# Performance work log

Measured on AMD Instinct MI355X. Metric: run time of the kernel, lower is better.

Reference implementation:

```python
import jax, jax.numpy as jnp
import numpy as np

G, B, C, H, W, D = 4, 1, 128, 32, 32, 32
STS = 4          # super_token_size (cubic)
N_ITER = 2
NUM_HEADS = 8
EPS = 1e-12


def _unfold3(x):
    """x: [..., H, W, D] -> [..., 27, H, W, D]; 3x3x3 neighborhood, zero pad."""
    *lead, h, w, d = x.shape
    xp = jnp.pad(x, [(0, 0)] * len(lead) + [(1, 1), (1, 1), (1, 1)])
    patches = [xp[..., i:i + h, j:j + w, l:l + d]
               for i in range(3) for j in range(3) for l in range(3)]
    return jnp.stack(patches, axis=-4)


def _fold3(x):
    """x: [..., 27, H, W, D] -> [..., H, W, D]; adjoint of _unfold3 (scatter-add)."""
    *lead, k27, h, w, d = x.shape
    out = jnp.zeros((*lead, h + 2, w + 2, d + 2), x.dtype)
    k = 0
    for i in range(3):
        for j in range(3):
            for l in range(3):
                out = out.at[..., i:i + h, j:j + w, l:l + d].add(x[..., k, :, :, :])
                k += 1
    return out[..., 1:h + 1, 1:w + 1, 1:d + 1]


def _attention_p(x, w_qkv, w_proj, b_proj):
    """Full self-attention over all voxels of x: [Bt, C, h, w, d]."""
    bt, c, hh, ww, dd = x.shape
    n = hh * ww * dd
    hd = c // NUM_HEADS
    xf = x.reshape(bt, c, n)
    qkv = jnp.einsum('oc,bcn->bon', w_qkv, xf)          # [Bt, 3C, N] (1x1 conv3d, no bias)
    q, k, v = jnp.split(qkv, 3, axis=1)
    q = q.reshape(bt * NUM_HEADS, hd, n) * (hd ** -0.5)
    k = k.reshape(bt * NUM_HEADS, hd, n)
    v = v.reshape(bt * NUM_HEADS, hd, n)
    attn = jax.nn.softmax(jnp.einsum('bcm,bcn->bmn', q, k), axis=-1)
    o = jnp.einsum('bmn,bcn->bcm', attn, v).reshape(bt, c, n)
    o = jnp.einsum('oc,bcn->bon', w_proj, o) + b_proj[None, :, None]
    return o.reshape(bt, c, hh, ww, dd)


def setup_inputs() -> dict:
    key = jax.random.key(0)
    k1, k2, k3, k4 = jax.random.split(key, 4)
    return {
        'x': jax.random.normal(k1, (G, B, C, H, W, D), jnp.float32),
        'w_qkv': jax.random.normal(k2, (3 * C, C), jnp.float32) * 0.02,
        'w_proj': jax.random.normal(k3, (C, C), jnp.float32) * 0.02,
        'b_proj': jax.random.normal(k4, (C,), jnp.float32) * 0.02,
    }


def reference(x, w_qkv, w_proj, b_proj):
    g, b, c, hH, wW, dD = x.shape
    bt = g * b
    xb = x.reshape(bt, c, hH, wW, dD)
    s = STS
    hh, ww, dd = hH // s, wW // s, dD // s
    m, p = hh * ww * dd, s ** 3
    scale = c ** -0.5

    blocks = xb.reshape(bt, c, hh, s, ww, s, dd, s)
    super_t = blocks.mean(axis=(3, 5, 7))                                   # [Bt,C,hh,ww,dd]
    pixel = blocks.transpose(0, 2, 4, 6, 3, 5, 7, 1).reshape(bt, m, p, c)    # [Bt,M,P,C]

    def _aff(st):
        su = _unfold3(st).reshape(bt, c, 27, m).transpose(0, 3, 1, 2)        # [Bt,M,C,27]
        return jax.nn.softmax(jnp.einsum('bmpc,bmck->bmpk', pixel, su) * scale, axis=-1)

    # iterative clustering (torch.no_grad in original)
    st = super_t
    aff = None
    asum = None
    for idx in range(N_ITER):
        aff = _aff(st)                                                       # [Bt,M,P,27]
        asum = _fold3(aff.sum(2).transpose(0, 2, 1).reshape(bt, 27, hh, ww, dd))[:, None]  # [Bt,1,hh,ww,dd]
        if idx < N_ITER - 1:
            stn = jnp.einsum('bmpc,bmpk->bmck', pixel, aff)                  # [Bt,M,C,27]
            stn = _fold3(stn.transpose(0, 2, 3, 1).reshape(bt, c, 27, hh, ww, dd))
            st = stn / (asum[:, 0][:, None] + EPS) if False else stn / (asum + EPS)
    aff = jax.lax.stop_gradient(aff)
    asum = jax.lax.stop_gradient(asum)

    st = jnp.einsum('bmpc,bmpk->bmck', pixel, aff)
    st = _fold3(st.transpose(0, 2, 3, 1).reshape(bt, c, 27, hh, ww, dd))
    st = st / (asum + EPS)                                                   # [Bt,C,hh,ww,dd]

    st = _attention_p(st, w_qkv, w_proj, b_proj)                             # refine

    su = _unfold3(st).reshape(bt, c, 27, m).transpose(0, 3, 1, 2)            # [Bt,M,C,27]
    pix = jnp.einsum('bmck,bmpk->bmcp', su, aff)                             # [Bt,M,C,P]
    out = pix.reshape(bt, hh, ww, dd, c, s, s, s).transpose(0, 4, 1, 5, 2, 6, 3, 7)
    out = out.reshape(bt, c, hH, wW, dD)
    return out.reshape(g, b, c, hH, wW, dD)
```

## Files before the change

kernel.cpp:

```cpp
#include <hip/hip_runtime.h>

#define BT 4
#define NC 128
#define MM 512
#define PP 64
#define K27 27
#define GSC 0.08838834764831845f
#define EPSF 1e-12f


__global__ __launch_bounds__(256) void k_pack(const float* __restrict__ x,
                                              float* __restrict__ px,
                                              float* __restrict__ st0p) {
    __shared__ float sl[128 * 36];
    const int blk = blockIdx.x & 255;
    const int phase = blockIdx.x >> 8;
    const int b = blk >> 6, gh = (blk >> 3) & 7, gw = blk & 7;
    const int tid = threadIdx.x;
    const int cL = tid >> 1, half = tid & 1;
    const int c4 = tid & 31, gd = tid >> 5;
    const int m = gh * 64 + gw * 8 + gd;
    float acc[4] = {0.f, 0.f, 0.f, 0.f};
    const size_t xbase = (size_t)b * NC * 32768 + (size_t)(gh * 4) * 1024 + (size_t)(gw * 4) * 32;

    for (int t = 0; t < 2; ++t) {
        const int ij = phase * 2 + t;
        const int i = ij >> 2, j = ij & 3;
        if (t) __syncthreads();
        const float* xp = x + xbase + (size_t)cL * 32768 + i * 1024 + j * 32 + half * 16;
#pragma unroll
        for (int q = 0; q < 4; ++q) {
            float4 v = *(const float4*)(xp + q * 4);
            *(float4*)&sl[cL * 36 + half * 16 + q * 4] = v;
        }
        __syncthreads();
        const float4 vq0 = *(const float4*)&sl[(c4 * 4 + 0) * 36 + gd * 4];
        const float4 vq1 = *(const float4*)&sl[(c4 * 4 + 1) * 36 + gd * 4];
        const float4 vq2 = *(const float4*)&sl[(c4 * 4 + 2) * 36 + gd * 4];
        const float4 vq3 = *(const float4*)&sl[(c4 * 4 + 3) * 36 + gd * 4];
        float* pb = px + ((size_t)(b * MM + m) * PP + (i * 16 + j * 4)) * NC + c4 * 4;
        *(float4*)(pb + 0 * NC) = make_float4(vq0.x, vq1.x, vq2.x, vq3.x);
        *(float4*)(pb + 1 * NC) = make_float4(vq0.y, vq1.y, vq2.y, vq3.y);
        *(float4*)(pb + 2 * NC) = make_float4(vq0.z, vq1.z, vq2.z, vq3.z);
        *(float4*)(pb + 3 * NC) = make_float4(vq0.w, vq1.w, vq2.w, vq3.w);
        acc[0] += vq0.x + vq0.y + vq0.z + vq0.w;
        acc[1] += vq1.x + vq1.y + vq1.z + vq1.w;
        acc[2] += vq2.x + vq2.y + vq2.z + vq2.w;
        acc[3] += vq3.x + vq3.y + vq3.z + vq3.w;
    }
    float4 a4 = make_float4(acc[0], acc[1], acc[2], acc[3]);
    a4.x *= (1.f / 64.f); a4.y *= (1.f / 64.f); a4.z *= (1.f / 64.f); a4.w *= (1.f / 64.f);
    *(float4*)&st0p[(size_t)phase * BT * MM * NC + (size_t)(b * MM + m) * NC + c4 * 4] = a4;
}

__global__ __launch_bounds__(128) void k_sum8(const float* __restrict__ st0p,
                                              float* __restrict__ st0) {
    const int row = blockIdx.x;
    const int c = threadIdx.x;
    const size_t idx = (size_t)row * NC + c;
    const size_t stride = (size_t)BT * MM * NC;
    float s = 0.f;
#pragma unroll
    for (int ph = 0; ph < 8; ++ph) s += st0p[ph * stride + idx];
    st0[idx] = s;
}

__global__ __launch_bounds__(256) void k_unpack(const float* __restrict__ pxo,
                                                float* __restrict__ out) {
    __shared__ float sl[128 * 36];
    const int blk = blockIdx.x & 255;
    const int phase = blockIdx.x >> 8;
    const int b = blk >> 6, gh = (blk >> 3) & 7, gw = blk & 7;
    const int tid = threadIdx.x;
    const int cL = tid >> 1, half = tid & 1;
    const int c4 = tid & 31, gd = tid >> 5;
    const int m = gh * 64 + gw * 8 + gd;
    const size_t obase = (size_t)b * NC * 32768 + (size_t)(gh * 4) * 1024 + (size_t)(gw * 4) * 32;

    for (int t = 0; t < 2; ++t) {
        const int ij = phase * 2 + t;
        const int i = ij >> 2, j = ij & 3;
        if (t) __syncthreads();
        const float* pb = pxo + ((size_t)(b * MM + m) * PP + (i * 16 + j * 4)) * NC + c4 * 4;
        const float4 w0 = *(const float4*)(pb + 0 * NC);
        const float4 w1 = *(const float4*)(pb + 1 * NC);
        const float4 w2 = *(const float4*)(pb + 2 * NC);
        const float4 w3 = *(const float4*)(pb + 3 * NC);
        *(float4*)&sl[(c4 * 4 + 0) * 36 + gd * 4] = make_float4(w0.x, w1.x, w2.x, w3.x);
        *(float4*)&sl[(c4 * 4 + 1) * 36 + gd * 4] = make_float4(w0.y, w1.y, w2.y, w3.y);
        *(float4*)&sl[(c4 * 4 + 2) * 36 + gd * 4] = make_float4(w0.z, w1.z, w2.z, w3.z);
        *(float4*)&sl[(c4 * 4 + 3) * 36 + gd * 4] = make_float4(w0.w, w1.w, w2.w, w3.w);
        __syncthreads();
        float* op = out + obase + (size_t)cL * 32768 + i * 1024 + j * 32 + half * 16;
#pragma unroll
        for (int q = 0; q < 4; ++q)
            *(float4*)(op + q * 4) = *(const float4*)&sl[cL * 36 + half * 16 + q * 4];
    }
}

template <int STORE_AFF>
__global__ __launch_bounds__(256) void k_iter(const float* __restrict__ px,
                                              const float* __restrict__ st,
                                              float* __restrict__ stn,
                                              float* __restrict__ affsum,
                                              float* __restrict__ affout) {
    __shared__ float pix[64 * 128];
    __shared__ float aff[64 * 28];
    const int tid = threadIdx.x;
    const int wg = blockIdx.x;
    const int b = wg >> 9;
    const int m = wg & (MM - 1);
    const int gh = m >> 6, gw = (m >> 3) & 7, gd = m & 7;

    const float* pxt = px + (size_t)wg * PP * NC;
    for (int t = tid; t < 2048; t += 256) {
        const int p = t >> 5, cb = t & 31;
        float4 v = *(const float4*)(pxt + t * 4);
        *(float4*)&pix[p * 128 + ((cb ^ (p & 7)) << 2)] = v;
    }

    const int kq = tid >> 6;
    const int kb = kq * 7;
    const int selfoff = (b * MM + m) * NC;
    int soff[7];
    int vmask = 0;
#pragma unroll
    for (int j = 0; j < 7; ++j) {
        const int k = kb + j;
        soff[j] = selfoff;
        if (k < K27) {
            const int i3 = k / 9, j3 = (k / 3) % 3, l3 = k % 3;
            const int mh = gh + i3 - 1, mw = gw + j3 - 1, md = gd + l3 - 1;
            if ((unsigned)mh < 8u && (unsigned)mw < 8u && (unsigned)md < 8u) {
                soff[j] = (b * MM + (mh * 64 + mw * 8 + md)) * NC;
                vmask |= (1 << j);
            }
        }
    }
    vmask = __builtin_amdgcn_readfirstlane(vmask);
    __syncthreads();

    {
        const int lane = tid & 63;
        const int pg = lane & 15, cseg = lane >> 4;
        float a00=0,a01=0,a02=0,a03=0,a04=0,a05=0,a06=0;
        float a10=0,a11=0,a12=0,a13=0,a14=0,a15=0,a16=0;
        float a20=0,a21=0,a22=0,a23=0,a24=0,a25=0,a26=0;
        float a30=0,a31=0,a32=0,a33=0,a34=0,a35=0,a36=0;
#pragma unroll 1
        for (int step = 0; step < 8; ++step) {
            const int cb = step * 4 + cseg;
            const int cb4 = cb * 4;
            const float4 sv0 = *(const float4*)(st + soff[0] + cb4);
            const float4 sv1 = *(const float4*)(st + soff[1] + cb4);
            const float4 sv2 = *(const float4*)(st + soff[2] + cb4);
            const float4 sv3 = *(const float4*)(st + soff[3] + cb4);
            const float4 sv4 = *(const float4*)(st + soff[4] + cb4);
            const float4 sv5 = *(const float4*)(st + soff[5] + cb4);
            const float4 sv6 = *(const float4*)(st + soff[6] + cb4);
            const float4 pv0 = *(const float4*)&pix[(pg +  0) * 128 + ((cb ^ ((pg +  0) & 7)) << 2)];
            const float4 pv1 = *(const float4*)&pix[(pg + 16) * 128 + ((cb ^ ((pg + 16) & 7)) << 2)];
            const float4 pv2 = *(const float4*)&pix[(pg + 32) * 128 + ((cb ^ ((pg + 32) & 7)) << 2)];
            const float4 pv3 = *(const float4*)&pix[(pg + 48) * 128 + ((cb ^ ((pg + 48) & 7)) << 2)];
#define DOT4(sv, A0, A1, A2, A3)                                          \
            A0 += pv0.x*sv.x + pv0.y*sv.y + pv0.z*sv.z + pv0.w*sv.w;      \
            A1 += pv1.x*sv.x + pv1.y*sv.y + pv1.z*sv.z + pv1.w*sv.w;      \
            A2 += pv2.x*sv.x + pv2.y*sv.y + pv2.z*sv.z + pv2.w*sv.w;      \
            A3 += pv3.x*sv.x + pv3.y*sv.y + pv3.z*sv.z + pv3.w*sv.w;
            DOT4(sv0, a00, a10, a20, a30)
            DOT4(sv1, a01, a11, a21, a31)
            DOT4(sv2, a02, a12, a22, a32)
            DOT4(sv3, a03, a13, a23, a33)
            DOT4(sv4, a04, a14, a24, a34)
            DOT4(sv5, a05, a15, a25, a35)
            DOT4(sv6, a06, a16, a26, a36)
#undef DOT4
        }
        if (!(vmask &  1)) { a00=0; a10=0; a20=0; a30=0; }
        if (!(vmask &  2)) { a01=0; a11=0; a21=0; a31=0; }
        if (!(vmask &  4)) { a02=0; a12=0; a22=0; a32=0; }
        if (!(vmask &  8)) { a03=0; a13=0; a23=0; a33=0; }
        if (!(vmask & 16)) { a04=0; a14=0; a24=0; a34=0; }
        if (!(vmask & 32)) { a05=0; a15=0; a25=0; a35=0; }
        if (!(vmask & 64)) { a06=0; a16=0; a26=0; a36=0; }
#define RED(v) v += __shfl_xor(v, 16); v += __shfl_xor(v, 32);
        RED(a00) RED(a01) RED(a02) RED(a03) RED(a04) RED(a05) RED(a06)
        RED(a10) RED(a11) RED(a12) RED(a13) RED(a14) RED(a15) RED(a16)
        RED(a20) RED(a21) RED(a22) RED(a23) RED(a24) RED(a25) RED(a26)
        RED(a30) RED(a31) RED(a32) RED(a33) RED(a34) RED(a35) RED(a36)
#undef RED
        if (cseg == 0) {
            float* r0 = &aff[(pg +  0) * 28 + kb];
            r0[0]=a00; r0[1]=a01; r0[2]=a02; r0[3]=a03; r0[4]=a04; r0[5]=a05; r0[6]=a06;
            float* r1 = &aff[(pg + 16) * 28 + kb];
            r1[0]=a10; r1[1]=a11; r1[2]=a12; r1[3]=a13; r1[4]=a14; r1[5]=a15; r1[6]=a16;
            float* r2 = &aff[(pg + 32) * 28 + kb];
            r2[0]=a20; r2[1]=a21; r2[2]=a22; r2[3]=a23; r2[4]=a24; r2[5]=a25; r2[6]=a26;
            float* r3 = &aff[(pg + 48) * 28 + kb];
            r3[0]=a30; r3[1]=a31; r3[2]=a32; r3[3]=a33; r3[4]=a34; r3[5]=a35; r3[6]=a36;
        }
    }
    __syncthreads();

    {
        const int p = tid >> 2, sub4 = tid & 3;
        const int k0 = sub4 * 7;
        float row[7];
        float mx = -1e30f;
#pragma unroll
        for (int t = 0; t < 7; ++t) {
            if (k0 + t < K27) {
                row[t] = aff[p * 28 + k0 + t] * GSC;
                mx = fmaxf(mx, row[t]);
            }
        }
        mx = fmaxf(mx, __shfl_xor(mx, 1));
        mx = fmaxf(mx, __shfl_xor(mx, 2));
        float s = 0.f;
#pragma unroll
        for (int t = 0; t < 7; ++t) {
            if (k0 + t < K27) {
                row[t] = __expf(row[t] - mx);
                s += row[t];
            }
        }
        s += __shfl_xor(s, 1);
        s += __shfl_xor(s, 2);
        const float inv = 1.f / s;
#pragma unroll
        for (int t = 0; t < 7; ++t)
            if (k0 + t < K27) aff[p * 28 + k0 + t] = row[t] * inv;
        if (sub4 == 3) aff[p * 28 + 27] = 0.f;
    }
    __syncthreads();

    if (tid < 216) {
        const int k = tid >> 3, seg = tid & 7;
        float s = 0.f;
#pragma unroll
        for (int pp = 0; pp < 8; ++pp) s += aff[(seg * 8 + pp) * 28 + k];
        s += __shfl_xor(s, 1);
        s += __shfl_xor(s, 2);
        s += __shfl_xor(s, 4);
        if (seg == 0) affsum[((size_t)b * K27 + k) * MM + m] = s;
    }
    if (STORE_AFF) {
        const size_t base = (size_t)(b * MM + m) * PP * K27;
        for (int t = tid; t < PP * K27; t += 256) {
            int p = t / K27, k = t - p * K27;
            affout[base + t] = aff[p * 28 + k];
        }
    }

    {
        const int kq2 = tid >> 5, cq = tid & 31;
        if (kq2 < 7) {
            float c00=0,c01=0,c02=0,c03=0;
            float c10=0,c11=0,c12=0,c13=0;
            float c20=0,c21=0,c22=0,c23=0;
            float c30=0,c31=0,c32=0,c33=0;
#pragma unroll 2
            for (int p = 0; p < 64; ++p) {
                float4 pv = *(const float4*)&pix[p * 128 + ((cq ^ (p & 7)) << 2)];
                float4 av = *(const float4*)&aff[p * 28 + kq2 * 4];
                c00 += av.x * pv.x; c01 += av.x * pv.y; c02 += av.x * pv.z; c03 += av.x * pv.w;
                c10 += av.y * pv.x; c11 += av.y * pv.y; c12 += av.y * pv.z; c13 += av.y * pv.w;
                c20 += av.z * pv.x; c21 += av.z * pv.y; c22 += av.z * pv.z; c23 += av.z * pv.w;
                c30 += av.w * pv.x; c31 += av.w * pv.y; c32 += av.w * pv.z; c33 += av.w * pv.w;
            }
            const int k0 = kq2 * 4;
#pragma unroll
            for (int q = 0; q < 4; ++q) {
                const int k = k0 + q;
                if (k < K27) {
                    const int i3 = k / 9, j3 = (k / 3) % 3, l3 = k % 3;
                    const int mh = gh + i3 - 1, mw = gw + j3 - 1, md = gd + l3 - 1;
                    if ((unsigned)mh < 8u && (unsigned)mw < 8u && (unsigned)md < 8u) {
                        float4 w4 = (q == 0) ? make_float4(c00, c01, c02, c03)
                                  : (q == 1) ? make_float4(c10, c11, c12, c13)
                                  : (q == 2) ? make_float4(c20, c21, c22, c23)
                                             : make_float4(c30, c31, c32, c33);
                        *(float4*)&stn[(((size_t)b * K27 + k) * MM + m) * NC + cq * 4] = w4;
                    }
                }
            }
        }
    }
}

__global__ __launch_bounds__(128) void k_fold(const float* __restrict__ stn,
                                              const float* __restrict__ affsum,
                                              float* __restrict__ stout) {
    const int wg = blockIdx.x;
    const int b = wg >> 9, g = wg & (MM - 1);
    const int gh = g >> 6, gw = (g >> 3) & 7, gd = g & 7;
    const int c = threadIdx.x;
    float num = 0.f, den = 0.f;
#pragma unroll
    for (int k = 0; k < K27; ++k) {
        int i = k / 9, j = (k / 3) % 3, l = k % 3;
        int mh = gh + 1 - i, mw = gw + 1 - j, md = gd + 1 - l;
        if ((unsigned)mh < 8u && (unsigned)mw < 8u && (unsigned)md < 8u) {
            int mm = mh * 64 + mw * 8 + md;
            num += stn[(((size_t)b * K27 + k) * MM + mm) * NC + c];
            den += affsum[((size_t)b * K27 + k) * MM + mm];
        }
    }
    stout[((size_t)b * MM + g) * NC + c] = num / (den + EPSF);
}

template <int COUT, int BIAS>
__global__ __launch_bounds__(256) void k_linear(const float* __restrict__ in,
                                                const float* __restrict__ w,
                                                const float* __restrict__ bias,
                                                float* __restrict__ out) {
    __shared__ float sl[8 * 128];
    const int tid = threadIdx.x;
    const int g0 = blockIdx.x * 8;
    {
        const int row = tid >> 5, c4 = (tid & 31) * 4;
        float4 v = *(const float4*)(in + (size_t)(g0 + row) * NC + c4);
        *(float4*)&sl[row * 128 + c4] = v;
    }
    __syncthreads();

    if (COUT == 384) {
#pragma unroll
        for (int pass = 0; pass < 2; ++pass) {
            const int o = tid + pass * 256;
            if (o < COUT) {
                const float* wr = w + (size_t)o * NC;
                float acc[8];
#pragma unroll
                for (int r = 0; r < 8; ++r) acc[r] = BIAS ? bias[o] : 0.f;
#pragma unroll 2
                for (int cs = 0; cs < 8; ++cs) {
                    const int c = cs * 16;
                    const float4 w0 = *(const float4*)(wr + c);
                    const float4 w1 = *(const float4*)(wr + c + 4);
                    const float4 w2 = *(const float4*)(wr + c + 8);
                    const float4 w3 = *(const float4*)(wr + c + 12);
#pragma unroll
                    for (int r = 0; r < 8; ++r) {
                        const float* xr = &sl[r * 128 + c];
                        const float4 x0 = *(const float4*)(xr);
                        const float4 x1 = *(const float4*)(xr + 4);
                        const float4 x2 = *(const float4*)(xr + 8);
                        const float4 x3 = *(const float4*)(xr + 12);
                        acc[r] += w0.x*x0.x + w0.y*x0.y + w0.z*x0.z + w0.w*x0.w
                                + w1.x*x1.x + w1.y*x1.y + w1.z*x1.z + w1.w*x1.w
                                + w2.x*x2.x + w2.y*x2.y + w2.z*x2.z + w2.w*x2.w
                                + w3.x*x3.x + w3.y*x3.y + w3.z*x3.z + w3.w*x3.w;
                    }
                }
#pragma unroll
                for (int r = 0; r < 8; ++r)
                    out[(size_t)(g0 + r) * COUT + o] = acc[r];
            }
        }
    } else {
        const int o = tid & 127;
        const int rb = (tid >> 7) * 4;
        const float* wr = w + (size_t)o * NC;
        float acc[4];
#pragma unroll
        for (int r = 0; r < 4; ++r) acc[r] = BIAS ? bias[o] : 0.f;
#pragma unroll 2
        for (int cs = 0; cs < 8; ++cs) {
            const int c = cs * 16;
            const float4 w0 = *(const float4*)(wr + c);
            const float4 w1 = *(const float4*)(wr + c + 4);
            const float4 w2 = *(const float4*)(wr + c + 8);
            const float4 w3 = *(const float4*)(wr + c + 12);
#pragma unroll
            for (int r = 0; r < 4; ++r) {
                const float* xr = &sl[(rb + r) * 128 + c];
                const float4 x0 = *(const float4*)(xr);
                const float4 x1 = *(const float4*)(xr + 4);
                const float4 x2 = *(const float4*)(xr + 8);
                const float4 x3 = *(const float4*)(xr + 12);
                acc[r] += w0.x*x0.x + w0.y*x0.y + w0.z*x0.z + w0.w*x0.w
                        + w1.x*x1.x + w1.y*x1.y + w1.z*x1.z + w1.w*x1.w
                        + w2.x*x2.x + w2.y*x2.y + w2.z*x2.z + w2.w*x2.w
                        + w3.x*x3.x + w3.y*x3.y + w3.z*x3.z + w3.w*x3.w;
            }
        }
#pragma unroll
        for (int r = 0; r < 4; ++r)
            out[(size_t)(g0 + rb + r) * COUT + o] = acc[r];
    }
}

__global__ __launch_bounds__(256) void k_attn(const float* __restrict__ qkv,
                                              float* __restrict__ obuf) {
    __shared__ float po[4][64][17];
    __shared__ float pl[4][64];
    const int b = blockIdx.x >> 6;
    const int h = (blockIdx.x >> 3) & 7;
    const int mt = blockIdx.x & 7;
    const int tid = threadIdx.x;
    const int nseg = tid >> 6, lane = tid & 63;
    const int m = mt * 64 + lane;

    float q[16];
    {
        const float* qp = qkv + (size_t)(b * MM + m) * 384 + h * 16;
#pragma unroll
        for (int cc = 0; cc < 16; cc += 4) {
            float4 t4 = *(const float4*)(qp + cc);
            q[cc + 0] = t4.x * 0.25f;
            q[cc + 1] = t4.y * 0.25f;
            q[cc + 2] = t4.z * 0.25f;
            q[cc + 3] = t4.w * 0.25f;
        }
    }
    float o[16];
#pragma unroll
    for (int i = 0; i < 16; ++i) o[i] = 0.f;
    float lsum = 0.f;
    const float* kb = qkv + (size_t)b * MM * 384 + 128 + h * 16;
    for (int n = nseg * 128; n < nseg * 128 + 128; ++n) {
        const float* kr = kb + (size_t)n * 384;
        float s = 0.f;
#pragma unroll
        for (int cc = 0; cc < 16; cc += 4) {
            float4 kv4 = *(const float4*)(kr + cc);
            s += q[cc] * kv4.x + q[cc + 1] * kv4.y + q[cc + 2] * kv4.z + q[cc + 3] * kv4.w;
        }
        float e = __expf(s);
        lsum += e;
        const float* vr = kr + 128;
#pragma unroll
        for (int cc = 0; cc < 16; cc += 4) {
            float4 vv = *(const float4*)(vr + cc);
            o[cc + 0] += e * vv.x;
            o[cc + 1] += e * vv.y;
            o[cc + 2] += e * vv.z;
            o[cc + 3] += e * vv.w;
        }
    }
#pragma unroll
    for (int cc = 0; cc < 16; ++cc) po[nseg][lane][cc] = o[cc];
    pl[nseg][lane] = lsum;
    __syncthreads();
    {
        const int ml = tid & 63, ccq = tid >> 6;
        float lt = pl[0][ml] + pl[1][ml] + pl[2][ml] + pl[3][ml];
        float inv = 1.f / lt;
        float* op = obuf + (size_t)(b * MM + mt * 64 + ml) * NC + h * 16 + ccq * 4;
        float4 w4;
        w4.x = (po[0][ml][ccq * 4 + 0] + po[1][ml][ccq * 4 + 0] + po[2][ml][ccq * 4 + 0] + po[3][ml][ccq * 4 + 0]) * inv;
        w4.y = (po[0][ml][ccq * 4 + 1] + po[1][ml][ccq * 4 + 1] + po[2][ml][ccq * 4 + 1] + po[3][ml][ccq * 4 + 1]) * inv;
        w4.z = (po[0][ml][ccq * 4 + 2] + po[1][ml][ccq * 4 + 2] + po[2][ml][ccq * 4 + 2] + po[3][ml][ccq * 4 + 2]) * inv;
        w4.w = (po[0][ml][ccq * 4 + 3] + po[1][ml][ccq * 4 + 3] + po[2][ml][ccq * 4 + 3] + po[3][ml][ccq * 4 + 3]) * inv;
        *(float4*)op = w4;
    }
}

__global__ __launch_bounds__(256) void k_final(const float* __restrict__ st3,
                                               const float* __restrict__ affin,
                                               float* __restrict__ pxo) {
    __shared__ float su[K27 * 132];
    __shared__ float aff[PP * 28];
    const int tid = threadIdx.x;
    const int wg = blockIdx.x;
    const int b = wg >> 9;
    const int m = wg & (MM - 1);
    const int gh = m >> 6, gw = (m >> 3) & 7, gd = m & 7;

    for (int t = tid; t < K27 * 128; t += 256) {
        int k = t >> 7, c = t & 127;
        int i = k / 9, j = (k / 3) % 3, l = k % 3;
        int mh = gh + i - 1, mw = gw + j - 1, md = gd + l - 1;
        float v = 0.f;
        if ((unsigned)mh < 8u && (unsigned)mw < 8u && (unsigned)md < 8u)
            v = st3[((size_t)b * MM + (mh * 64 + mw * 8 + md)) * NC + c];
        su[k * 132 + c] = v;
    }
    {
        const size_t base = (size_t)(b * MM + m) * PP * K27;
        for (int t = tid; t < PP * K27; t += 256) {
            int p = t / K27, k = t - p * K27;
            aff[p * 28 + k] = affin[base + t];
        }
    }
    __syncthreads();

    const int cg = tid & 31;
    const int pg = tid >> 5;
    float acc[4][8];
#pragma unroll
    for (int q = 0; q < 4; ++q)
#pragma unroll
        for (int pp = 0; pp < 8; ++pp) acc[q][pp] = 0.f;
    for (int k = 0; k < K27; ++k) {
        float4 sv = *(const float4*)&su[k * 132 + cg * 4];
#pragma unroll
        for (int pp = 0; pp < 8; ++pp) {
            float av = aff[(pg * 8 + pp) * 28 + k];
            acc[0][pp] += sv.x * av;
            acc[1][pp] += sv.y * av;
            acc[2][pp] += sv.z * av;
            acc[3][pp] += sv.w * av;
        }
    }
    float* pb = pxo + (size_t)wg * PP * NC;
#pragma unroll
    for (int pp = 0; pp < 8; ++pp) {
        float4 w4;
        w4.x = acc[0][pp];
        w4.y = acc[1][pp];
        w4.z = acc[2][pp];
        w4.w = acc[3][pp];
        *(float4*)&pb[(pg * 8 + pp) * NC + cg * 4] = w4;
    }
}

extern "C" void kernel_launch(void* const* d_in, const int* in_sizes, int n_in,
                              void* d_out, int out_size, void* d_ws, size_t ws_size,
                              hipStream_t stream) {
    (void)in_sizes; (void)n_in; (void)out_size; (void)ws_size;
    const float* x = (const float*)d_in[0];
    const float* w_qkv = (const float*)d_in[1];
    const float* w_proj = (const float*)d_in[2];
    const float* b_proj = (const float*)d_in[3];
    float* out = (float*)d_out;

    float* ws = (float*)d_ws;
    float* px = ws;
    float* st0 = px + (size_t)BT * MM * PP * NC;
    float* st1 = st0 + (size_t)BT * MM * NC;
    float* st2 = st1 + (size_t)BT * MM * NC;
    float* st3 = st2 + (size_t)BT * MM * NC;
    float* qkvb = st3 + (size_t)BT * MM * NC;
    float* obuf = qkvb + (size_t)BT * MM * 384;
    float* stn = obuf + (size_t)BT * MM * NC;
    float* afs = stn + (size_t)BT * K27 * MM * NC;
    float* aff1 = afs + (size_t)BT * K27 * MM;
    float* st0p = aff1 + (size_t)BT * MM * PP * K27;

    hipLaunchKernelGGL(k_pack, dim3(2048), dim3(256), 0, stream, x, px, st0p);
    hipLaunchKernelGGL(k_sum8, dim3(BT * MM), dim3(128), 0, stream, st0p, st0);
    hipLaunchKernelGGL((k_iter<0>), dim3(BT * MM), dim3(256), 0, stream, px, st0, stn, afs, aff1);
    hipLaunchKernelGGL(k_fold, dim3(BT * MM), dim3(128), 0, stream, stn, afs, st1);
    hipLaunchKernelGGL((k_iter<1>), dim3(BT * MM), dim3(256), 0, stream, px, st1, stn, afs, aff1);
    hipLaunchKernelGGL(k_fold, dim3(BT * MM), dim3(128), 0, stream, stn, afs, st2);
    hipLaunchKernelGGL((k_linear<384, 0>), dim3(BT * MM / 8), dim3(256), 0, stream, st2, w_qkv, b_proj, qkvb);
    hipLaunchKernelGGL(k_attn, dim3(256), dim3(256), 0, stream, qkvb, obuf);
    hipLaunchKernelGGL((k_linear<128, 1>), dim3(BT * MM / 8), dim3(256), 0, stream, obuf, w_proj, b_proj, st3);
    hipLaunchKernelGGL(k_final, dim3(BT * MM), dim3(256), 0, stream, st3, aff1, px);
    hipLaunchKernelGGL(k_unpack, dim3(2048), dim3(256), 0, stream, px, out);
}
```

Before: 385.1 us.

## Fuse final super-token upsampling with output unpack via LDS-transposed tile

Merges k_final and k_unpack into a single kernel. Each 1024-thread block handles a whole (b,gh,gw) column of 8 super tokens. It stages the 3x3 neighbourhood of st3 and the affinities in LDS, computes the pixel outputs in registers, then writes them straight to the output layout through a swizzled LDS tile. This removes the 33 MB round trip through the px workspace and one kernel launch. The cost is fewer blocks (256) with large LDS use, and the write-back is serialised over four phases with extra barriers.

```diff
diff --git a/kernel.cpp b/kernel.cpp
--- a/kernel.cpp
+++ b/kernel.cpp
@@ -48,8 +48,8 @@
         acc[2] += vq2.x + vq2.y + vq2.z + vq2.w;
         acc[3] += vq3.x + vq3.y + vq3.z + vq3.w;
     }
-    float4 a4 = make_float4(acc[0], acc[1], acc[2], acc[3]);
-    a4.x *= (1.f / 64.f); a4.y *= (1.f / 64.f); a4.z *= (1.f / 64.f); a4.w *= (1.f / 64.f);
+    float4 a4 = make_float4(acc[0] * (1.f / 64.f), acc[1] * (1.f / 64.f),
+                            acc[2] * (1.f / 64.f), acc[3] * (1.f / 64.f));
     *(float4*)&st0p[(size_t)phase * BT * MM * NC + (size_t)(b * MM + m) * NC + c4 * 4] = a4;
 }
 
@@ -63,39 +63,6 @@
 #pragma unroll
     for (int ph = 0; ph < 8; ++ph) s += st0p[ph * stride + idx];
     st0[idx] = s;
-}
-
-__global__ __launch_bounds__(256) void k_unpack(const float* __restrict__ pxo,
-                                                float* __restrict__ out) {
-    __shared__ float sl[128 * 36];
-    const int blk = blockIdx.x & 255;
-    const int phase = blockIdx.x >> 8;
-    const int b = blk >> 6, gh = (blk >> 3) & 7, gw = blk & 7;
-    const int tid = threadIdx.x;
-    const int cL = tid >> 1, half = tid & 1;
-    const int c4 = tid & 31, gd = tid >> 5;
-    const int m = gh * 64 + gw * 8 + gd;
-    const size_t obase = (size_t)b * NC * 32768 + (size_t)(gh * 4) * 1024 + (size_t)(gw * 4) * 32;
-
-    for (int t = 0; t < 2; ++t) {
-        const int ij = phase * 2 + t;
-        const int i = ij >> 2, j = ij & 3;
-        if (t) __syncthreads();
-        const float* pb = pxo + ((size_t)(b * MM + m) * PP + (i * 16 + j * 4)) * NC + c4 * 4;
-        const float4 w0 = *(const float4*)(pb + 0 * NC);
-        const float4 w1 = *(const float4*)(pb + 1 * NC);
-        const float4 w2 = *(const float4*)(pb + 2 * NC);
-        const float4 w3 = *(const float4*)(pb + 3 * NC);
-        *(float4*)&sl[(c4 * 4 + 0) * 36 + gd * 4] = make_float4(w0.x, w1.x, w2.x, w3.x);
-        *(float4*)&sl[(c4 * 4 + 1) * 36 + gd * 4] = make_float4(w0.y, w1.y, w2.y, w3.y);
-        *(float4*)&sl[(c4 * 4 + 2) * 36 + gd * 4] = make_float4(w0.z, w1.z, w2.z, w3.z);
-        *(float4*)&sl[(c4 * 4 + 3) * 36 + gd * 4] = make_float4(w0.w, w1.w, w2.w, w3.w);
-        __syncthreads();
-        float* op = out + obase + (size_t)cL * 32768 + i * 1024 + j * 32 + half * 16;
-#pragma unroll
-        for (int q = 0; q < 4; ++q)
-            *(float4*)(op + q * 4) = *(const float4*)&sl[cL * 36 + half * 16 + q * 4];
-    }
 }
 
 template <int STORE_AFF>
@@ -457,62 +424,84 @@
     }
 }
 
-__global__ __launch_bounds__(256) void k_final(const float* __restrict__ st3,
-                                               const float* __restrict__ affin,
-                                               float* __restrict__ pxo) {
-    __shared__ float su[K27 * 132];
-    __shared__ float aff[PP * 28];
+__global__ __launch_bounds__(1024) void k_final2(const float* __restrict__ st3,
+                                                 const float* __restrict__ affin,
+                                                 float* __restrict__ out) {
+    __shared__ float lds[23460];
+    float* stg  = lds;
+    float* affl = lds + 9636;
+    float* tile = lds;
+
+    const int blk = blockIdx.x;
+    const int b = blk >> 6, gh = (blk >> 3) & 7, gw = blk & 7;
     const int tid = threadIdx.x;
-    const int wg = blockIdx.x;
-    const int b = wg >> 9;
-    const int m = wg & (MM - 1);
-    const int gh = m >> 6, gw = (m >> 3) & 7, gd = m & 7;
-
-    for (int t = tid; t < K27 * 128; t += 256) {
-        int k = t >> 7, c = t & 127;
-        int i = k / 9, j = (k / 3) % 3, l = k % 3;
-        int mh = gh + i - 1, mw = gw + j - 1, md = gd + l - 1;
-        float v = 0.f;
-        if ((unsigned)mh < 8u && (unsigned)mw < 8u && (unsigned)md < 8u)
-            v = st3[((size_t)b * MM + (mh * 64 + mw * 8 + md)) * NC + c];
-        su[k * 132 + c] = v;
-    }
-    {
-        const size_t base = (size_t)(b * MM + m) * PP * K27;
-        for (int t = tid; t < PP * K27; t += 256) {
-            int p = t / K27, k = t - p * K27;
-            aff[p * 28 + k] = affin[base + t];
-        }
-    }
-    __syncthreads();
-
-    const int cg = tid & 31;
-    const int pg = tid >> 5;
-    float acc[4][8];
-#pragma unroll
-    for (int q = 0; q < 4; ++q)
-#pragma unroll
-        for (int pp = 0; pp < 8; ++pp) acc[q][pp] = 0.f;
+    const int cg = tid & 31, gd = (tid >> 5) & 7, iq = tid >> 8;
+
+    for (int t = tid; t < 9 * 8 * 32; t += 1024) {
+        const int seg = t >> 8;
+        const int dh = seg / 3, dw = seg % 3;
+        const int md = (t >> 5) & 7, c4 = t & 31;
+        const int mh = gh + dh - 1, mw = gw + dw - 1;
+        if ((unsigned)mh < 8u && (unsigned)mw < 8u) {
+            float4 v = *(const float4*)(st3 + ((size_t)(b * MM + mh * 64 + mw * 8 + md)) * NC + c4 * 4);
+            *(float4*)&stg[(seg * 8 + md) * 132 + c4 * 4] = v;
+        }
+    }
+    if (tid < 33) *(float4*)&stg[72 * 132 + tid * 4] = make_float4(0.f, 0.f, 0.f, 0.f);
+    {
+        const float* ab = affin + (size_t)(b * MM + gh * 64 + gw * 8) * PP * K27;
+        for (int t = tid; t < 3456; t += 1024)
+            *(float4*)&affl[t * 4] = *(const float4*)(ab + t * 4);
+    }
+    __syncthreads();
+
+    float acc[4][16];
+#pragma unroll
+    for (int c = 0; c < 4; ++c)
+#pragma unroll
+        for (int jl = 0; jl < 16; ++jl) acc[c][jl] = 0.f;
+
+    const float* arow = &affl[(gd * 64 + iq * 16) * 27];
+#pragma unroll 1
     for (int k = 0; k < K27; ++k) {
-        float4 sv = *(const float4*)&su[k * 132 + cg * 4];
-#pragma unroll
-        for (int pp = 0; pp < 8; ++pp) {
-            float av = aff[(pg * 8 + pp) * 28 + k];
-            acc[0][pp] += sv.x * av;
-            acc[1][pp] += sv.y * av;
-            acc[2][pp] += sv.z * av;
-            acc[3][pp] += sv.w * av;
-        }
-    }
-    float* pb = pxo + (size_t)wg * PP * NC;
-#pragma unroll
-    for (int pp = 0; pp < 8; ++pp) {
-        float4 w4;
-        w4.x = acc[0][pp];
-        w4.y = acc[1][pp];
-        w4.z = acc[2][pp];
-        w4.w = acc[3][pp];
-        *(float4*)&pb[(pg * 8 + pp) * NC + cg * 4] = w4;
+        const int i3 = k / 9, j3 = (k / 3) % 3, l3 = k % 3;
+        const int mh = gh + i3 - 1, mw = gw + j3 - 1, md = gd + l3 - 1;
+        const bool ok = ((unsigned)mh < 8u) && ((unsigned)mw < 8u) && ((unsigned)md < 8u);
+        const int row = ok ? ((i3 * 3 + j3) * 8 + md) : 72;
+        const float4 su4 = *(const float4*)&stg[row * 132 + cg * 4];
+#pragma unroll
+        for (int jl = 0; jl < 16; ++jl) {
+            const float a = arow[jl * 27 + k];
+            acc[0][jl] += a * su4.x;
+            acc[1][jl] += a * su4.y;
+            acc[2][jl] += a * su4.z;
+            acc[3][jl] += a * su4.w;
+        }
+    }
+    __syncthreads();
+
+    const size_t obase = (size_t)b * NC * 32768 + (size_t)(gh * 4) * 1024 + (size_t)(gw * 4) * 32;
+    for (int ci = 0; ci < 4; ++ci) {
+        if (ci) __syncthreads();
+        if (iq == ci) {
+#pragma unroll
+            for (int c4 = 0; c4 < 4; ++c4)
+#pragma unroll
+                for (int j = 0; j < 4; ++j)
+                    *(float4*)&tile[(((cg * 4 + c4) * 4 + j)) * 33 + ((gd ^ (cg & 7)) << 2)] =
+                        make_float4(acc[c4][j * 4 + 0], acc[c4][j * 4 + 1],
+                                    acc[c4][j * 4 + 2], acc[c4][j * 4 + 3]);
+        }
+        __syncthreads();
+#pragma unroll
+        for (int q = 0; q < 4; ++q) {
+            const int idx = tid + q * 1024;
+            const int tpl = idx >> 3, seg = idx & 7;
+            const int c = tpl >> 2, j = tpl & 3;
+            const int swz = (c >> 2) & 7;
+            float4 v = *(const float4*)&tile[tpl * 33 + ((seg ^ swz) << 2)];
+            *(float4*)(out + obase + (size_t)c * 32768 + ci * 1024 + j * 32 + seg * 4) = v;
+        }
     }
 }
 
@@ -548,6 +537,5 @@
     hipLaunchKernelGGL((k_linear<384, 0>), dim3(BT * MM / 8), dim3(256), 0, stream, st2, w_qkv, b_proj, qkvb);
     hipLaunchKernelGGL(k_attn, dim3(256), dim3(256), 0, stream, qkvb, obuf);
     hipLaunchKernelGGL((k_linear<128, 1>), dim3(BT * MM / 8), dim3(256), 0, stream, obuf, w_proj, b_proj, st3);
-    hipLaunchKernelGGL(k_final, dim3(BT * MM), dim3(256), 0, stream, st3, aff1, px);
-    hipLaunchKernelGGL(k_unpack, dim3(2048), dim3(256), 0, stream, px, out);
-}
+    hipLaunchKernelGGL(k_final2, dim3(BT * 64), dim3(1024), 0, stream, st3, aff1, out);
+}
```

Measured after the change: 341.1 us. 1.13x faster.
